# Kernel optimization log

Measured on AMD Instinct MI355X. Metric: run time of the kernel, lower is better.

## Reference

```python
import jax, jax.numpy as jnp
import numpy as np

D = 65
CHUNK = 64
K = 64
SCALE = D ** (-0.5)

def gelu(x):
    return jax.nn.gelu(x, approximate=False)  # torch nn.GELU default is exact erf

def setup_inputs() -> dict:
    key = jax.random.key(0)
    ks = jax.random.split(key, 16)
    B, N = 32, 16384
    s = SCALE
    return {
        "x": jax.random.normal(ks[0], (B, N, D), jnp.float32),
        # query_gen: Linear(D,D) -> GELU -> Linear(D, K*D)
        "Wq1": jax.random.normal(ks[1], (D, D), jnp.float32) * s,
        "bq1": jnp.zeros((D,), jnp.float32),
        "Wq2": jax.random.normal(ks[2], (D, K * D), jnp.float32) * s,
        "bq2": jnp.zeros((K * D,), jnp.float32),
        "Wk": jax.random.normal(ks[3], (D, D), jnp.float32) * s,
        "bk": jnp.zeros((D,), jnp.float32),
        "Wv": jax.random.normal(ks[4], (D, D), jnp.float32) * s,
        "bv": jnp.zeros((D,), jnp.float32),
        "cross_q": jax.random.normal(ks[5], (1, D), jnp.float32) * s,
        "pos_enc": jax.random.normal(ks[6], (1, CHUNK, D), jnp.float32) * s,
        "Wr": jax.random.normal(ks[7], (D, D), jnp.float32) * (1.0 / np.sqrt(D)),
        "br": jnp.zeros((D,), jnp.float32),
        "gamma": jnp.ones((D,), jnp.float32),
        "beta": jnp.zeros((D,), jnp.float32),
    }

def reference(x, Wq1, bq1, Wq2, bq2, Wk, bk, Wv, bv, cross_q, pos_enc, Wr, br, gamma, beta):
    B, N, d = x.shape
    nb = N // CHUNK  # N chosen divisible by CHUNK -> mask is all True, pad branch skipped

    # global average (mask all-ones => plain mean over N)
    gavg = jnp.mean(x, axis=1)  # [B, D]

    # queries: MLP on global average, reshape to [B, K, D], scaled
    q = (gelu(gavg @ Wq1 + bq1) @ Wq2 + bq2).reshape(B, K, d) * SCALE

    # keys / values: Linear + GELU, chunked, + positional encoding per chunk
    keys = gelu(x @ Wk + bk).reshape(B, nb, CHUNK, d) + pos_enc[None]      # [B,nb,C,D]
    values = gelu(x @ Wv + bv).reshape(B, nb, CHUNK, d) + pos_enc[None]    # [B,nb,C,D]

    # block-local attention (mask is all-True, masked_fill is a no-op)
    scores = jnp.einsum('bkd,bncd->bnkc', q, keys) * SCALE                 # [B,nb,K,C]
    w = jax.nn.softmax(scores, axis=-1)                                    # dropout = eval-mode identity
    blk = jnp.einsum('bnkc,bncd->bnkd', w, values)                         # [B,nb,K,D]
    blk = jnp.transpose(blk, (0, 2, 1, 3))                                 # [B,K,nb,D]

    # cross-block attention with a single learned query
    cs = jnp.einsum('d,bknd->bkn', cross_q[0], blk) * SCALE                # [B,K,nb]
    cw = jax.nn.softmax(cs, axis=-1)
    compressed = jnp.einsum('bkn,bknd->bkd', cw, blk)                      # [B,K,D]

    # residual + LayerNorm
    compressed = compressed + (gavg @ Wr + br)[:, None, :]
    mu = jnp.mean(compressed, axis=-1, keepdims=True)
    var = jnp.var(compressed, axis=-1, keepdims=True)
    return (compressed - mu) * jax.lax.rsqrt(var + 1e-5) * gamma + beta
```

## Files before the change

### kernel.cpp

```cpp
#include <hip/hip_runtime.h>
#include <hip/hip_bf16.h>

#define BATCH 32
#define NSEQ  16384
#define DDIM  65
#define CHUNK 64
#define KQ    64
#define NBLK  256
#define SCALE 0.12403473458920847f

typedef __bf16 bf16x8 __attribute__((ext_vector_type(8)));
typedef float  f32x4  __attribute__((ext_vector_type(4)));
#define MFMA16(a, b, c) __builtin_amdgcn_mfma_f32_16x16x32_bf16(a, b, c, 0, 0, 0)

#define BLK_ROWSTRIDE 72
#define BLK_CHUNKSTRIDE (64 * 72)
#define BLK_BSTRIDE ((size_t)NBLK * 64 * 72)

__device__ __forceinline__ float gelu_exact(float v) {
    return 0.5f * v * (1.0f + erff(v * 0.7071067811865476f));
}

__device__ __forceinline__ float gelu_tanh(float x) {
    float x2 = x * x;
    float t  = 0.7978845608028654f * x * fmaf(0.044715f, x2, 1.0f);
    float e  = __expf(2.0f * t);
    float th = 1.0f - 2.0f * __builtin_amdgcn_rcpf(e + 1.0f);
    return 0.5f * x * (1.0f + th);
}

__global__ __launch_bounds__(320) void k_gavg(const float* __restrict__ x,
                                              float* __restrict__ partial,
                                              const float* __restrict__ Wk,
                                              const float* __restrict__ Wv,
                                              __bf16* __restrict__ WkT,
                                              __bf16* __restrict__ WvT) {
    const int tid = threadIdx.x;
    if (blockIdx.y == 32) {
        const int i = blockIdx.x * 320 + tid;
        const int m = i / 5120;
        const int j = i - m * 5120;
        const int d = j >> 6, e = j & 63;
        const float* W = m ? Wv : Wk;
        __bf16* T = m ? WvT : WkT;
        T[(size_t)d * 64 + e] = (d < DDIM) ? (__bf16)W[e * DDIM + d]
                                           : (__bf16)0.0f;
        return;
    }
    const int s = blockIdx.x;
    const int b = blockIdx.y;
    const int g = tid / 65;
    const int j = tid - g * 65;
    const bool active = tid < 260;
    float acc[4] = {0.f, 0.f, 0.f, 0.f};
    if (active) {
        const float4* p = (const float4*)(x + (size_t)b * NSEQ * DDIM
                                            + (size_t)s * 512 * DDIM);
        #pragma unroll 8
        for (int it = 0; it < 32; ++it) {
            const float4 v = p[(it * 4 + g) * 65 + j];
            acc[0] += v.x; acc[1] += v.y; acc[2] += v.z; acc[3] += v.w;
        }
    }
    __shared__ float lds[4][65][4];
    if (active) {
        lds[g][j][0] = acc[0]; lds[g][j][1] = acc[1];
        lds[g][j][2] = acc[2]; lds[g][j][3] = acc[3];
    }
    __syncthreads();
    if (tid < DDIM) {
        float a = 0.f;
        #pragma unroll
        for (int rr = 0; rr < 4; ++rr) {
            const int f = tid + 65 * rr;
            const int jj = f >> 2, ee = f & 3;
            a += lds[0][jj][ee] + lds[1][jj][ee]
               + lds[2][jj][ee] + lds[3][jj][ee];
        }
        partial[((size_t)b * 32 + s) * DDIM + tid] = a;
    }
}

__global__ __launch_bounds__(256) void k_qgen1(const float* __restrict__ partial,
    const float* __restrict__ Wq1, const float* __restrict__ bq1,
    const float* __restrict__ Wr,  const float* __restrict__ br,
    float* __restrict__ h_out, float* __restrict__ r_out) {
    const int b = blockIdx.x, tid = threadIdx.x;
    __shared__ float g[DDIM];
    if (tid < DDIM) {
        float a = 0.f;
        const float* p = partial + (size_t)b * 32 * DDIM + tid;
        #pragma unroll 8
        for (int s = 0; s < 32; ++s) a += p[s * DDIM];
        g[tid] = a * (1.0f / 16384.0f);
    }
    __syncthreads();
    if (tid < DDIM) {
        float a = bq1[tid];
        for (int e = 0; e < DDIM; ++e) a += g[e] * Wq1[e * DDIM + tid];
        h_out[b * DDIM + tid] = gelu_exact(a);
    } else if (tid >= 128 && tid < 128 + DDIM) {
        const int d = tid - 128;
        float a = br[d];
        for (int e = 0; e < DDIM; ++e) a += g[e] * Wr[e * DDIM + d];
        r_out[b * DDIM + d] = a;
    }
}

__global__ __launch_bounds__(256) void k_qgen2(const float* __restrict__ h_in,
    const float* __restrict__ Wq2, const float* __restrict__ bq2,
    __bf16* __restrict__ qbf, float* __restrict__ q64) {
    const int b = blockIdx.y, tid = threadIdx.x;
    const int o = blockIdx.x * 256 + tid;
    __shared__ float h[DDIM];
    if (tid < DDIM) h[tid] = h_in[b * DDIM + tid];
    __syncthreads();
    if (o >= KQ * DDIM) return;
    float a = bq2[o];
    #pragma unroll 13
    for (int e = 0; e < DDIM; ++e) a += h[e] * Wq2[e * (KQ * DDIM) + o];
    a *= SCALE;
    const int k = o / DDIM, d = o - k * DDIM;
    if (d < 64) qbf[(size_t)b * 4096 + k * 64 + d] = (__bf16)a;
    else        q64[b * 64 + k] = a;
}

__global__ __launch_bounds__(256) void k_attn(const float* __restrict__ x,
    const __bf16* __restrict__ qbf, const float* __restrict__ q64,
    const __bf16* __restrict__ WkT, const __bf16* __restrict__ WvT,
    const float* __restrict__ Wk, const float* __restrict__ bkb,
    const float* __restrict__ Wv, const float* __restrict__ bvb,
    const float* __restrict__ pos, const float* __restrict__ cq,
    __bf16* __restrict__ blk_out, float* __restrict__ cs_out) {
    const int nb = blockIdx.x;
    const int b  = blockIdx.y;
    const int tid = threadIdx.x;
    const int lane = tid & 63, w = tid >> 6;
    const int l16 = lane & 15, quad = lane >> 4;

    __shared__ __align__(16) __bf16 keys[64 * 72];
    __shared__ __align__(16) __bf16 valsT[64 * 72];
    __shared__ float vals64[64];
    __shared__ float xs64[64];

    __bf16* blk_row = blk_out + (size_t)b * BLK_BSTRIDE
                              + (size_t)nb * BLK_CHUNKSTRIDE;

    float wk64v[5], wv64v[5], bkv[5], bvv[5], posv[5][4];
    {
        #pragma unroll
        for (int nt = 0; nt < 5; ++nt) {
            const int d = nt * 16 + l16;
            const int dc = d > 64 ? 64 : d;
            wk64v[nt] = Wk[64 * DDIM + dc];
            wv64v[nt] = Wv[64 * DDIM + dc];
            bkv[nt]   = bkb[dc];
            bvv[nt]   = bvb[dc];
            #pragma unroll
            for (int r = 0; r < 4; ++r)
                posv[nt][r] = pos[(w * 16 + quad * 4 + r) * DDIM + dc];
        }
    }

    {
        const int c = tid >> 2, g = tid & 3;
        const float* xrow = x + ((size_t)b * NSEQ + (size_t)nb * CHUNK + c) * DDIM;
        __bf16* dst = keys + c * 72;
        #pragma unroll
        for (int j = 0; j < 16; ++j)
            dst[g + 4 * j] = (__bf16)xrow[g + 4 * j];
        if (g == 0) xs64[c] = xrow[64];
    }
    __syncthreads();

    {
        const __bf16* arow = keys + (w * 16 + l16) * 72 + quad * 8;
        bf16x8 a0 = *(const bf16x8*)arow;
        bf16x8 a1 = *(const bf16x8*)(arow + 32);
        f32x4 ak[5], av[5];
        const f32x4 z = {0.f, 0.f, 0.f, 0.f};
        #pragma unroll
        for (int nt = 0; nt < 5; ++nt) {
            const __bf16* bkr = WkT + (nt * 16 + l16) * 64 + quad * 8;
            const __bf16* bvr = WvT + (nt * 16 + l16) * 64 + quad * 8;
            ak[nt] = MFMA16(a0, *(const bf16x8*)bkr, z);
            ak[nt] = MFMA16(a1, *(const bf16x8*)(bkr + 32), ak[nt]);
            av[nt] = MFMA16(a0, *(const bf16x8*)bvr, z);
            av[nt] = MFMA16(a1, *(const bf16x8*)(bvr + 32), av[nt]);
        }
        const float4 xe4 = *(const float4*)(xs64 + w * 16 + quad * 4);
        const float xe[4] = {xe4.x, xe4.y, xe4.z, xe4.w};
        #pragma unroll
        for (int nt = 0; nt < 5; ++nt) {
            const int d = nt * 16 + l16;
            if (d <= 64) {
                #pragma unroll
                for (int r = 0; r < 4; ++r) {
                    const int c = w * 16 + quad * 4 + r;
                    const float pv = posv[nt][r];
                    const float kvv = gelu_tanh(fmaf(xe[r], wk64v[nt], ak[nt][r]) + bkv[nt]) + pv;
                    const float vvv = gelu_tanh(fmaf(xe[r], wv64v[nt], av[nt][r]) + bvv[nt]) + pv;
                    keys[c * 72 + d] = (__bf16)kvv;
                    if (d < 64) valsT[d * 72 + c] = (__bf16)vvv;
                    else        vals64[c] = vvv;
                }
            }
        }
    }
    __syncthreads();

    float st[4][4];
    float inv[4];
    {
        const __bf16* aq = qbf + (size_t)b * 4096 + (w * 16 + l16) * 64 + quad * 8;
        bf16x8 qa0 = *(const bf16x8*)aq;
        bf16x8 qa1 = *(const bf16x8*)(aq + 32);
        const f32x4 z = {0.f, 0.f, 0.f, 0.f};
        const float4 q4 = *(const float4*)(q64 + b * 64 + w * 16 + quad * 4);
        const float q64k[4] = {q4.x, q4.y, q4.z, q4.w};
        #pragma unroll
        for (int nt = 0; nt < 4; ++nt) {
            const __bf16* kb = keys + (nt * 16 + l16) * 72 + quad * 8;
            f32x4 sacc = MFMA16(qa0, *(const bf16x8*)kb, z);
            sacc = MFMA16(qa1, *(const bf16x8*)(kb + 32), sacc);
            const float k64c = (float)keys[(nt * 16 + l16) * 72 + 64];
            #pragma unroll
            for (int r = 0; r < 4; ++r)
                st[nt][r] = fmaf(q64k[r], k64c, sacc[r]) * SCALE;
        }
        float mr[4], sum[4];
        #pragma unroll
        for (int r = 0; r < 4; ++r) {
            float m = fmaxf(fmaxf(st[0][r], st[1][r]), fmaxf(st[2][r], st[3][r]));
            m = fmaxf(m, __shfl_xor(m, 1));
            m = fmaxf(m, __shfl_xor(m, 2));
            m = fmaxf(m, __shfl_xor(m, 4));
            m = fmaxf(m, __shfl_xor(m, 8));
            mr[r] = m;
            sum[r] = 0.f;
        }
        #pragma unroll
        for (int nt = 0; nt < 4; ++nt)
            #pragma unroll
            for (int r = 0; r < 4; ++r) {
                st[nt][r] = __expf(st[nt][r] - mr[r]);
                sum[r] += st[nt][r];
            }
        #pragma unroll
        for (int r = 0; r < 4; ++r) {
            float s = sum[r];
            s += __shfl_xor(s, 1);
            s += __shfl_xor(s, 2);
            s += __shfl_xor(s, 4);
            s += __shfl_xor(s, 8);
            inv[r] = __builtin_amdgcn_rcpf(s);
        }
    }
    __syncthreads();

    float csr[4];
    {
        #pragma unroll
        for (int nt = 0; nt < 4; ++nt)
            #pragma unroll
            for (int r = 0; r < 4; ++r)
                keys[(w * 16 + quad * 4 + r) * 72 + nt * 16 + l16] =
                    (__bf16)(st[nt][r] * inv[r]);
        float v64l[4];
        #pragma unroll
        for (int nt = 0; nt < 4; ++nt) v64l[nt] = vals64[nt * 16 + l16];
        const float cq64 = cq[64];
        #pragma unroll
        for (int r = 0; r < 4; ++r) {
            float o = st[0][r] * v64l[0];
            o = fmaf(st[1][r], v64l[1], o);
            o = fmaf(st[2][r], v64l[2], o);
            o = fmaf(st[3][r], v64l[3], o);
            o += __shfl_xor(o, 1);
            o += __shfl_xor(o, 2);
            o += __shfl_xor(o, 4);
            o += __shfl_xor(o, 8);
            csr[r] = 0.f;
            if (l16 == 0) {
                const float o64 = o * inv[r];
                const int k = w * 16 + quad * 4 + r;
                bf16x8 v8;
                #pragma unroll
                for (int i2 = 0; i2 < 8; ++i2) v8[i2] = (__bf16)0.0f;
                v8[0] = (__bf16)o64;
                *(bf16x8*)(blk_row + k * BLK_ROWSTRIDE + 64) = v8;
                csr[r] = o64 * cq64;
            }
        }
    }

    {
        const __bf16* pr = keys + (w * 16 + l16) * 72 + quad * 8;
        bf16x8 pa0 = *(const bf16x8*)pr;
        bf16x8 pa1 = *(const bf16x8*)(pr + 32);
        const f32x4 z = {0.f, 0.f, 0.f, 0.f};
        #pragma unroll
        for (int nt = 0; nt < 4; ++nt) {
            const __bf16* vb = valsT + (nt * 16 + l16) * 72 + quad * 8;
            f32x4 o = MFMA16(pa0, *(const bf16x8*)vb, z);
            o = MFMA16(pa1, *(const bf16x8*)(vb + 32), o);
            const int d = nt * 16 + l16;
            const float cqd = cq[d];
            #pragma unroll
            for (int r = 0; r < 4; ++r) {
                const int k = w * 16 + quad * 4 + r;
                blk_row[k * BLK_ROWSTRIDE + d] = (__bf16)o[r];
                csr[r] = fmaf(o[r], cqd, csr[r]);
            }
        }
        #pragma unroll
        for (int r = 0; r < 4; ++r) {
            float v = csr[r];
            v += __shfl_xor(v, 1);
            v += __shfl_xor(v, 2);
            v += __shfl_xor(v, 4);
            v += __shfl_xor(v, 8);
            if (l16 == 0) {
                const int k = w * 16 + quad * 4 + r;
                cs_out[((size_t)b * KQ + k) * NBLK + nb] = v * SCALE;
            }
        }
    }
}

__global__ __launch_bounds__(256) void k_cross(
    const __bf16* __restrict__ blk, const float* __restrict__ cs,
    const float* __restrict__ rres, const float* __restrict__ gamma,
    const float* __restrict__ beta, float* __restrict__ out) {
    const int bk_ = blockIdx.x;
    const int b = bk_ >> 6, k = bk_ & 63;
    const int tid = threadIdx.x;
    const int w = tid >> 6, lane = tid & 63;

    __shared__ float ew[NBLK];
    __shared__ float wredA[4];
    __shared__ float lred[252][8];
    __shared__ float vv[DDIM];
    __shared__ float stats[2];

    const float v = cs[(size_t)bk_ * NBLK + tid];
    float m = v;
    for (int off = 32; off; off >>= 1) m = fmaxf(m, __shfl_down(m, off));
    if (lane == 0) wredA[w] = m;
    __syncthreads();
    m = fmaxf(fmaxf(wredA[0], wredA[1]), fmaxf(wredA[2], wredA[3]));
    const float e = __expf(v - m);
    ew[tid] = e;
    float s = e;
    for (int off = 32; off; off >>= 1) s += __shfl_down(s, off);
    __syncthreads();
    if (lane == 0) wredA[w] = s;
    __syncthreads();
    const float inv = 1.0f / (wredA[0] + wredA[1] + wredA[2] + wredA[3]);

    const int g = tid / 9, seg = tid - g * 9;
    float acc[8] = {0.f, 0.f, 0.f, 0.f, 0.f, 0.f, 0.f, 0.f};
    if (tid < 252) {
        const __bf16* base = blk + (size_t)b * BLK_BSTRIDE
                                 + k * BLK_ROWSTRIDE + seg * 8;
        #pragma unroll 2
        for (int it = 0; it < 10; ++it) {
            const int r = it * 28 + g;
            if (r < NBLK) {
                bf16x8 vx = *(const bf16x8*)(base + (size_t)r * BLK_CHUNKSTRIDE);
                const float wg = ew[r];
                #pragma unroll
                for (int i2 = 0; i2 < 8; ++i2)
                    acc[i2] = fmaf(wg, (float)vx[i2], acc[i2]);
            }
        }
        #pragma unroll
        for (int i2 = 0; i2 < 8; ++i2) lred[tid][i2] = acc[i2];
    }
    __syncthreads();
    if (tid < 72) {
        const int sg = tid >> 3, i2 = tid & 7;
        float a = 0.f;
        #pragma unroll 7
        for (int gg = 0; gg < 28; ++gg) a += lred[gg * 9 + sg][i2];
        const int d = sg * 8 + i2;
        if (d < DDIM) vv[d] = a * inv + rres[b * DDIM + d];
    }
    __syncthreads();
    if (tid < 64) {
        float a  = vv[tid] + (tid == 0 ? vv[64] : 0.f);
        float sq = vv[tid] * vv[tid] + (tid == 0 ? vv[64] * vv[64] : 0.f);
        for (int off = 32; off; off >>= 1) {
            a  += __shfl_down(a, off);
            sq += __shfl_down(sq, off);
        }
        if (tid == 0) {
            const float mu  = a * (1.0f / DDIM);
            const float var = sq * (1.0f / DDIM) - mu * mu;
            stats[0] = mu;
            stats[1] = rsqrtf(var + 1e-5f);
        }
    }
    __syncthreads();
    if (tid < DDIM) {
        out[(size_t)bk_ * DDIM + tid] =
            (vv[tid] - stats[0]) * stats[1] * gamma[tid] + beta[tid];
    }
}

extern "C" void kernel_launch(void* const* d_in, const int* in_sizes, int n_in,
                              void* d_out, int out_size, void* d_ws, size_t ws_size,
                              hipStream_t stream) {
    const float* x    = (const float*)d_in[0];
    const float* Wq1  = (const float*)d_in[1];
    const float* bq1  = (const float*)d_in[2];
    const float* Wq2  = (const float*)d_in[3];
    const float* bq2  = (const float*)d_in[4];
    const float* Wk   = (const float*)d_in[5];
    const float* bk   = (const float*)d_in[6];
    const float* Wv   = (const float*)d_in[7];
    const float* bv   = (const float*)d_in[8];
    const float* cq   = (const float*)d_in[9];
    const float* pos  = (const float*)d_in[10];
    const float* Wr   = (const float*)d_in[11];
    const float* br   = (const float*)d_in[12];
    const float* gamma= (const float*)d_in[13];
    const float* beta = (const float*)d_in[14];
    float* out = (float*)d_out;

    char* w8 = (char*)d_ws;
    __bf16* blk     = (__bf16*)w8;
    float*  partial = (float*)w8;
    float*  rres    = (float*)(w8 + 75497472);
    float*  q64     = (float*)(w8 + 75505792);
    float*  hbuf    = (float*)(w8 + 75513984);
    float*  cs      = (float*)(w8 + 75522304);
    __bf16* qbf     = (__bf16*)(w8 + 77619456);
    __bf16* WkT     = (__bf16*)(w8 + 77881600);
    __bf16* WvT     = (__bf16*)(w8 + 77891840);

    k_gavg<<<dim3(32, 33), 320, 0, stream>>>(x, partial, Wk, Wv, WkT, WvT);
    k_qgen1<<<BATCH, 256, 0, stream>>>(partial, Wq1, bq1, Wr, br, hbuf, rres);
    k_qgen2<<<dim3(17, BATCH), 256, 0, stream>>>(hbuf, Wq2, bq2, qbf, q64);
    k_attn<<<dim3(NBLK, BATCH), 256, 0, stream>>>(x, qbf, q64, WkT, WvT,
                                                  Wk, bk, Wv, bv, pos, cq,
                                                  blk, cs);
    k_cross<<<BATCH * KQ, 256, 0, stream>>>(blk, cs, rres, gamma, beta, out);
}
```

Measured before the change: 380.9 us.

## Coalesce x loads with float4 and stage block output through LDS

The chunk of x is now read as contiguous float4 vectors and scattered into the bf16 LDS tile, replacing strided per-element loads. The block attention output is staged in shared memory (reusing valsT) and then written to global memory with coalesced 16-byte vector stores instead of scattered 2-byte stores. cross_q values are hoisted into registers. This adds two extra barriers and index arithmetic with divide-by-65 tricks.

```diff
diff --git a/kernel.cpp b/kernel.cpp
--- a/kernel.cpp
+++ b/kernel.cpp
@@ -146,7 +146,8 @@
     __bf16* blk_row = blk_out + (size_t)b * BLK_BSTRIDE
                               + (size_t)nb * BLK_CHUNKSTRIDE;
 
-    float wk64v[5], wv64v[5], bkv[5], bvv[5], posv[5][4];
+    float wk64v[5], wv64v[5], bkv[5], bvv[5], posv[5][4], cqv[4];
+    float cq64;
     {
         #pragma unroll
         for (int nt = 0; nt < 5; ++nt) {
@@ -160,16 +161,30 @@
             for (int r = 0; r < 4; ++r)
                 posv[nt][r] = pos[(w * 16 + quad * 4 + r) * DDIM + dc];
         }
-    }
-
-    {
-        const int c = tid >> 2, g = tid & 3;
-        const float* xrow = x + ((size_t)b * NSEQ + (size_t)nb * CHUNK + c) * DDIM;
-        __bf16* dst = keys + c * 72;
-        #pragma unroll
-        for (int j = 0; j < 16; ++j)
-            dst[g + 4 * j] = (__bf16)xrow[g + 4 * j];
-        if (g == 0) xs64[c] = xrow[64];
+        #pragma unroll
+        for (int nt = 0; nt < 4; ++nt) cqv[nt] = cq[nt * 16 + l16];
+        cq64 = cq[64];
+    }
+
+    {
+        const float4* xf4 = (const float4*)(x + ((size_t)b * NSEQ
+                                                 + (size_t)nb * CHUNK) * DDIM);
+        #pragma unroll
+        for (int ii = 0; ii < 5; ++ii) {
+            const int F = ii * 256 + tid;
+            if (ii < 4 || tid < 16) {
+                const float4 v = xf4[F];
+                const int idx0 = 4 * F;
+                int c = (idx0 * 4033) >> 18;
+                int e = idx0 - c * 65;
+                const float vv[4] = {v.x, v.y, v.z, v.w};
+                #pragma unroll
+                for (int i = 0; i < 4; ++i) {
+                    if (e == 64) { xs64[c] = vv[i]; c += 1; e = 0; }
+                    else         { keys[c * 72 + e] = (__bf16)vv[i]; e += 1; }
+                }
+            }
+        }
     }
     __syncthreads();
 
@@ -258,7 +273,7 @@
     }
     __syncthreads();
 
-    float csr[4];
+    float csr[4], o64r[4];
     {
         #pragma unroll
         for (int nt = 0; nt < 4; ++nt)
@@ -269,7 +284,6 @@
         float v64l[4];
         #pragma unroll
         for (int nt = 0; nt < 4; ++nt) v64l[nt] = vals64[nt * 16 + l16];
-        const float cq64 = cq[64];
         #pragma unroll
         for (int r = 0; r < 4; ++r) {
             float o = st[0][r] * v64l[0];
@@ -280,37 +294,49 @@
             o += __shfl_xor(o, 2);
             o += __shfl_xor(o, 4);
             o += __shfl_xor(o, 8);
-            csr[r] = 0.f;
+            o64r[r] = 0.f;
+            csr[r]  = 0.f;
             if (l16 == 0) {
-                const float o64 = o * inv[r];
+                o64r[r] = o * inv[r];
+                csr[r]  = o64r[r] * cq64;
+            }
+        }
+    }
+
+    {
+        const __bf16* pr = keys + (w * 16 + l16) * 72 + quad * 8;
+        bf16x8 pa0 = *(const bf16x8*)pr;
+        bf16x8 pa1 = *(const bf16x8*)(pr + 32);
+        const f32x4 z = {0.f, 0.f, 0.f, 0.f};
+        f32x4 o[4];
+        #pragma unroll
+        for (int nt = 0; nt < 4; ++nt) {
+            const __bf16* vb = valsT + (nt * 16 + l16) * 72 + quad * 8;
+            o[nt] = MFMA16(pa0, *(const bf16x8*)vb, z);
+            o[nt] = MFMA16(pa1, *(const bf16x8*)(vb + 32), o[nt]);
+        }
+        __syncthreads();
+        __bf16* outl = valsT;
+        #pragma unroll
+        for (int nt = 0; nt < 4; ++nt) {
+            const int d = nt * 16 + l16;
+            const float cqd = cqv[nt];
+            #pragma unroll
+            for (int r = 0; r < 4; ++r) {
+                const int k = w * 16 + quad * 4 + r;
+                outl[k * 72 + d] = (__bf16)o[nt][r];
+                csr[r] = fmaf(o[nt][r], cqd, csr[r]);
+            }
+        }
+        if (l16 == 0) {
+            #pragma unroll
+            for (int r = 0; r < 4; ++r) {
                 const int k = w * 16 + quad * 4 + r;
                 bf16x8 v8;
                 #pragma unroll
                 for (int i2 = 0; i2 < 8; ++i2) v8[i2] = (__bf16)0.0f;
-                v8[0] = (__bf16)o64;
-                *(bf16x8*)(blk_row + k * BLK_ROWSTRIDE + 64) = v8;
-                csr[r] = o64 * cq64;
-            }
-        }
-    }
-
-    {
-        const __bf16* pr = keys + (w * 16 + l16) * 72 + quad * 8;
-        bf16x8 pa0 = *(const bf16x8*)pr;
-        bf16x8 pa1 = *(const bf16x8*)(pr + 32);
-        const f32x4 z = {0.f, 0.f, 0.f, 0.f};
-        #pragma unroll
-        for (int nt = 0; nt < 4; ++nt) {
-            const __bf16* vb = valsT + (nt * 16 + l16) * 72 + quad * 8;
-            f32x4 o = MFMA16(pa0, *(const bf16x8*)vb, z);
-            o = MFMA16(pa1, *(const bf16x8*)(vb + 32), o);
-            const int d = nt * 16 + l16;
-            const float cqd = cq[d];
-            #pragma unroll
-            for (int r = 0; r < 4; ++r) {
-                const int k = w * 16 + quad * 4 + r;
-                blk_row[k * BLK_ROWSTRIDE + d] = (__bf16)o[r];
-                csr[r] = fmaf(o[r], cqd, csr[r]);
+                v8[0] = (__bf16)o64r[r];
+                *(bf16x8*)(outl + k * 72 + 64) = v8;
             }
         }
         #pragma unroll
@@ -325,6 +351,12 @@
                 cs_out[((size_t)b * KQ + k) * NBLK + nb] = v * SCALE;
             }
         }
+        __syncthreads();
+        const bf16x8* src = (const bf16x8*)outl;
+        bf16x8* dst = (bf16x8*)blk_row;
+        dst[tid]       = src[tid];
+        dst[tid + 256] = src[tid + 256];
+        if (tid < 64) dst[tid + 512] = src[tid + 512];
     }
 }
 
```

Result: no change. 382.4 us (+0.4%).

## Process one chunk per wavefront in attention kernel to remove block barriers

Applied to the files above, without the earlier changes.

The attention kernel now gives each 64-lane wavefront a whole 64-token chunk, with two chunks per 128-thread block, instead of splitting one chunk over four wavefronts. Each wave loops over four 16-row tiles, so all __syncthreads barriers disappear and only wave-private LDS is used. x is loaded straight from global memory into MFMA operand registers rather than staged through shared memory. In exchange each wave does four times the serial work and holds a 64-entry score array in registers, which may raise register pressure and reduce occupancy or latency hiding.

```diff
diff --git a/kernel.cpp b/kernel.cpp
--- a/kernel.cpp
+++ b/kernel.cpp
@@ -27,6 +27,12 @@
     float e  = __expf(2.0f * t);
     float th = 1.0f - 2.0f * __builtin_amdgcn_rcpf(e + 1.0f);
     return 0.5f * x * (1.0f + th);
+}
+
+__device__ __forceinline__ f32x4 ld4u(const float* p) {
+    f32x4 v;
+    __builtin_memcpy(&v, p, 16);
+    return v;
 }
 
 __global__ __launch_bounds__(320) void k_gavg(const float* __restrict__ x,
@@ -125,113 +131,119 @@
     else        q64[b * 64 + k] = a;
 }
 
-__global__ __launch_bounds__(256) void k_attn(const float* __restrict__ x,
+__global__ __launch_bounds__(128) void k_attn(const float* __restrict__ x,
     const __bf16* __restrict__ qbf, const float* __restrict__ q64,
     const __bf16* __restrict__ WkT, const __bf16* __restrict__ WvT,
     const float* __restrict__ Wk, const float* __restrict__ bkb,
     const float* __restrict__ Wv, const float* __restrict__ bvb,
     const float* __restrict__ pos, const float* __restrict__ cq,
     __bf16* __restrict__ blk_out, float* __restrict__ cs_out) {
-    const int nb = blockIdx.x;
-    const int b  = blockIdx.y;
-    const int tid = threadIdx.x;
-    const int lane = tid & 63, w = tid >> 6;
-    const int l16 = lane & 15, quad = lane >> 4;
-
-    __shared__ __align__(16) __bf16 keys[64 * 72];
-    __shared__ __align__(16) __bf16 valsT[64 * 72];
-    __shared__ float vals64[64];
-    __shared__ float xs64[64];
-
+    const int tid  = threadIdx.x;
+    const int w    = tid >> 6, lane = tid & 63;
+    const int l16  = lane & 15, quad = lane >> 4;
+    const int nb   = blockIdx.x * 2 + w;
+    const int b    = blockIdx.y;
+
+    __shared__ __align__(16) __bf16 ksh[2][64 * 72];
+    __shared__ __align__(16) __bf16 vsh[2][64 * 72];
+    __shared__ float v64sh[2][64];
+    __bf16* K   = ksh[w];
+    __bf16* VT  = vsh[w];
+    float*  V64 = v64sh[w];
+
+    const float* xc = x + ((size_t)b * NSEQ + (size_t)nb * CHUNK) * DDIM;
     __bf16* blk_row = blk_out + (size_t)b * BLK_BSTRIDE
                               + (size_t)nb * BLK_CHUNKSTRIDE;
-
-    float wk64v[5], wv64v[5], bkv[5], bvv[5], posv[5][4];
-    {
+    const f32x4 z = {0.f, 0.f, 0.f, 0.f};
+
+    float wk64v[5], wv64v[5], bkv[5], bvv[5], cqv[4];
+    #pragma unroll
+    for (int nt = 0; nt < 5; ++nt) {
+        const int d  = nt * 16 + l16;
+        const int dc = d > 64 ? 64 : d;
+        wk64v[nt] = Wk[64 * DDIM + dc];
+        wv64v[nt] = Wv[64 * DDIM + dc];
+        bkv[nt]   = bkb[dc];
+        bvv[nt]   = bvb[dc];
+    }
+    #pragma unroll
+    for (int nt = 0; nt < 4; ++nt) cqv[nt] = cq[nt * 16 + l16];
+    const float cq64 = cq[64];
+
+    #pragma unroll
+    for (int mt = 0; mt < 4; ++mt) {
+        const float* xrow = xc + (mt * 16 + l16) * DDIM;
+        const f32x4 xa = ld4u(xrow + quad * 8);
+        const f32x4 xb = ld4u(xrow + quad * 8 + 4);
+        const f32x4 xc2 = ld4u(xrow + 32 + quad * 8);
+        const f32x4 xd = ld4u(xrow + 36 + quad * 8);
+        bf16x8 a0, a1;
+        #pragma unroll
+        for (int i = 0; i < 4; ++i) {
+            a0[i]     = (__bf16)xa[i];
+            a0[4 + i] = (__bf16)xb[i];
+            a1[i]     = (__bf16)xc2[i];
+            a1[4 + i] = (__bf16)xd[i];
+        }
+        f32x4 aK[5], aV[5];
         #pragma unroll
         for (int nt = 0; nt < 5; ++nt) {
-            const int d = nt * 16 + l16;
-            const int dc = d > 64 ? 64 : d;
-            wk64v[nt] = Wk[64 * DDIM + dc];
-            wv64v[nt] = Wv[64 * DDIM + dc];
-            bkv[nt]   = bkb[dc];
-            bvv[nt]   = bvb[dc];
-            #pragma unroll
-            for (int r = 0; r < 4; ++r)
-                posv[nt][r] = pos[(w * 16 + quad * 4 + r) * DDIM + dc];
-        }
-    }
-
-    {
-        const int c = tid >> 2, g = tid & 3;
-        const float* xrow = x + ((size_t)b * NSEQ + (size_t)nb * CHUNK + c) * DDIM;
-        __bf16* dst = keys + c * 72;
-        #pragma unroll
-        for (int j = 0; j < 16; ++j)
-            dst[g + 4 * j] = (__bf16)xrow[g + 4 * j];
-        if (g == 0) xs64[c] = xrow[64];
-    }
-    __syncthreads();
-
-    {
-        const __bf16* arow = keys + (w * 16 + l16) * 72 + quad * 8;
-        bf16x8 a0 = *(const bf16x8*)arow;
-        bf16x8 a1 = *(const bf16x8*)(arow + 32);
-        f32x4 ak[5], av[5];
-        const f32x4 z = {0.f, 0.f, 0.f, 0.f};
-        #pragma unroll
-        for (int nt = 0; nt < 5; ++nt) {
-            const __bf16* bkr = WkT + (nt * 16 + l16) * 64 + quad * 8;
-            const __bf16* bvr = WvT + (nt * 16 + l16) * 64 + quad * 8;
-            ak[nt] = MFMA16(a0, *(const bf16x8*)bkr, z);
-            ak[nt] = MFMA16(a1, *(const bf16x8*)(bkr + 32), ak[nt]);
-            av[nt] = MFMA16(a0, *(const bf16x8*)bvr, z);
-            av[nt] = MFMA16(a1, *(const bf16x8*)(bvr + 32), av[nt]);
-        }
-        const float4 xe4 = *(const float4*)(xs64 + w * 16 + quad * 4);
-        const float xe[4] = {xe4.x, xe4.y, xe4.z, xe4.w};
+            const __bf16* bk0 = WkT + (nt * 16 + l16) * 64 + quad * 8;
+            const __bf16* bv0 = WvT + (nt * 16 + l16) * 64 + quad * 8;
+            aK[nt] = MFMA16(a0, *(const bf16x8*)bk0, z);
+            aK[nt] = MFMA16(a1, *(const bf16x8*)(bk0 + 32), aK[nt]);
+            aV[nt] = MFMA16(a0, *(const bf16x8*)bv0, z);
+            aV[nt] = MFMA16(a1, *(const bf16x8*)(bv0 + 32), aV[nt]);
+        }
+        float xe[4];
+        #pragma unroll
+        for (int r = 0; r < 4; ++r)
+            xe[r] = xc[(mt * 16 + quad * 4 + r) * DDIM + 64];
         #pragma unroll
         for (int nt = 0; nt < 5; ++nt) {
             const int d = nt * 16 + l16;
             if (d <= 64) {
                 #pragma unroll
                 for (int r = 0; r < 4; ++r) {
-                    const int c = w * 16 + quad * 4 + r;
-                    const float pv = posv[nt][r];
-                    const float kvv = gelu_tanh(fmaf(xe[r], wk64v[nt], ak[nt][r]) + bkv[nt]) + pv;
-                    const float vvv = gelu_tanh(fmaf(xe[r], wv64v[nt], av[nt][r]) + bvv[nt]) + pv;
-                    keys[c * 72 + d] = (__bf16)kvv;
-                    if (d < 64) valsT[d * 72 + c] = (__bf16)vvv;
-                    else        vals64[c] = vvv;
+                    const int c = mt * 16 + quad * 4 + r;
+                    const float pv = pos[c * DDIM + d];
+                    const float kv = gelu_tanh(fmaf(xe[r], wk64v[nt], aK[nt][r]) + bkv[nt]) + pv;
+                    const float vv = gelu_tanh(fmaf(xe[r], wv64v[nt], aV[nt][r]) + bvv[nt]) + pv;
+                    K[c * 72 + d] = (__bf16)kv;
+                    if (d < 64) VT[d * 72 + c] = (__bf16)vv;
+                    else        V64[c] = vv;
                 }
             }
         }
     }
-    __syncthreads();
-
-    float st[4][4];
-    float inv[4];
-    {
-        const __bf16* aq = qbf + (size_t)b * 4096 + (w * 16 + l16) * 64 + quad * 8;
-        bf16x8 qa0 = *(const bf16x8*)aq;
-        bf16x8 qa1 = *(const bf16x8*)(aq + 32);
-        const f32x4 z = {0.f, 0.f, 0.f, 0.f};
-        const float4 q4 = *(const float4*)(q64 + b * 64 + w * 16 + quad * 4);
-        const float q64k[4] = {q4.x, q4.y, q4.z, q4.w};
-        #pragma unroll
-        for (int nt = 0; nt < 4; ++nt) {
-            const __bf16* kb = keys + (nt * 16 + l16) * 72 + quad * 8;
+
+    float st[4][4][4];
+    #pragma unroll
+    for (int mtk = 0; mtk < 4; ++mtk) {
+        const __bf16* aq = qbf + (size_t)b * 4096 + (mtk * 16 + l16) * 64 + quad * 8;
+        const bf16x8 qa0 = *(const bf16x8*)aq;
+        const bf16x8 qa1 = *(const bf16x8*)(aq + 32);
+        const f32x4 q4 = *(const f32x4*)(q64 + b * 64 + mtk * 16 + quad * 4);
+        #pragma unroll
+        for (int ntc = 0; ntc < 4; ++ntc) {
+            const __bf16* kb = K + (ntc * 16 + l16) * 72 + quad * 8;
             f32x4 sacc = MFMA16(qa0, *(const bf16x8*)kb, z);
             sacc = MFMA16(qa1, *(const bf16x8*)(kb + 32), sacc);
-            const float k64c = (float)keys[(nt * 16 + l16) * 72 + 64];
+            const float k64c = (float)K[(ntc * 16 + l16) * 72 + 64];
             #pragma unroll
             for (int r = 0; r < 4; ++r)
-                st[nt][r] = fmaf(q64k[r], k64c, sacc[r]) * SCALE;
-        }
-        float mr[4], sum[4];
+                st[mtk][ntc][r] = fmaf(q4[r], k64c, sacc[r]) * SCALE;
+        }
+    }
+
+    float o64r[4][4];
+    #pragma unroll
+    for (int mtk = 0; mtk < 4; ++mtk) {
+        float mr[4], sum[4], inv[4];
         #pragma unroll
         for (int r = 0; r < 4; ++r) {
-            float m = fmaxf(fmaxf(st[0][r], st[1][r]), fmaxf(st[2][r], st[3][r]));
+            float m = fmaxf(fmaxf(st[mtk][0][r], st[mtk][1][r]),
+                            fmaxf(st[mtk][2][r], st[mtk][3][r]));
             m = fmaxf(m, __shfl_xor(m, 1));
             m = fmaxf(m, __shfl_xor(m, 2));
             m = fmaxf(m, __shfl_xor(m, 4));
@@ -240,11 +252,11 @@
             sum[r] = 0.f;
         }
         #pragma unroll
-        for (int nt = 0; nt < 4; ++nt)
+        for (int ntc = 0; ntc < 4; ++ntc)
             #pragma unroll
             for (int r = 0; r < 4; ++r) {
-                st[nt][r] = __expf(st[nt][r] - mr[r]);
-                sum[r] += st[nt][r];
+                st[mtk][ntc][r] = __expf(st[mtk][ntc][r] - mr[r]);
+                sum[r] += st[mtk][ntc][r];
             }
         #pragma unroll
         for (int r = 0; r < 4; ++r) {
@@ -255,62 +267,61 @@
             s += __shfl_xor(s, 8);
             inv[r] = __builtin_amdgcn_rcpf(s);
         }
-    }
-    __syncthreads();
-
-    float csr[4];
-    {
-        #pragma unroll
-        for (int nt = 0; nt < 4; ++nt)
+        #pragma unroll
+        for (int ntc = 0; ntc < 4; ++ntc)
             #pragma unroll
             for (int r = 0; r < 4; ++r)
-                keys[(w * 16 + quad * 4 + r) * 72 + nt * 16 + l16] =
-                    (__bf16)(st[nt][r] * inv[r]);
+                K[(mtk * 16 + quad * 4 + r) * 72 + ntc * 16 + l16] =
+                    (__bf16)(st[mtk][ntc][r] * inv[r]);
         float v64l[4];
         #pragma unroll
-        for (int nt = 0; nt < 4; ++nt) v64l[nt] = vals64[nt * 16 + l16];
-        const float cq64 = cq[64];
+        for (int ntc = 0; ntc < 4; ++ntc) v64l[ntc] = V64[ntc * 16 + l16];
         #pragma unroll
         for (int r = 0; r < 4; ++r) {
-            float o = st[0][r] * v64l[0];
-            o = fmaf(st[1][r], v64l[1], o);
-            o = fmaf(st[2][r], v64l[2], o);
-            o = fmaf(st[3][r], v64l[3], o);
+            float o = st[mtk][0][r] * v64l[0];
+            o = fmaf(st[mtk][1][r], v64l[1], o);
+            o = fmaf(st[mtk][2][r], v64l[2], o);
+            o = fmaf(st[mtk][3][r], v64l[3], o);
             o += __shfl_xor(o, 1);
             o += __shfl_xor(o, 2);
             o += __shfl_xor(o, 4);
             o += __shfl_xor(o, 8);
-            csr[r] = 0.f;
-            if (l16 == 0) {
-                const float o64 = o * inv[r];
-                const int k = w * 16 + quad * 4 + r;
+            o64r[mtk][r] = (l16 == 0) ? o * inv[r] : 0.f;
+        }
+    }
+
+    #pragma unroll
+    for (int mtk = 0; mtk < 4; ++mtk) {
+        const __bf16* pr = K + (mtk * 16 + l16) * 72 + quad * 8;
+        const bf16x8 pa0 = *(const bf16x8*)pr;
+        const bf16x8 pa1 = *(const bf16x8*)(pr + 32);
+        float csr[4];
+        #pragma unroll
+        for (int r = 0; r < 4; ++r)
+            csr[r] = (l16 == 0) ? o64r[mtk][r] * cq64 : 0.f;
+        #pragma unroll
+        for (int nt = 0; nt < 4; ++nt) {
+            const __bf16* vb = VT + (nt * 16 + l16) * 72 + quad * 8;
+            f32x4 o = MFMA16(pa0, *(const bf16x8*)vb, z);
+            o = MFMA16(pa1, *(const bf16x8*)(vb + 32), o);
+            const int d = nt * 16 + l16;
+            const float cqd = cqv[nt];
+            #pragma unroll
+            for (int r = 0; r < 4; ++r) {
+                const int k = mtk * 16 + quad * 4 + r;
+                blk_row[k * BLK_ROWSTRIDE + d] = (__bf16)o[r];
+                csr[r] = fmaf(o[r], cqd, csr[r]);
+            }
+        }
+        if (l16 == 0) {
+            #pragma unroll
+            for (int r = 0; r < 4; ++r) {
+                const int k = mtk * 16 + quad * 4 + r;
                 bf16x8 v8;
                 #pragma unroll
                 for (int i2 = 0; i2 < 8; ++i2) v8[i2] = (__bf16)0.0f;
-                v8[0] = (__bf16)o64;
+                v8[0] = (__bf16)o64r[mtk][r];
                 *(bf16x8*)(blk_row + k * BLK_ROWSTRIDE + 64) = v8;
-                csr[r] = o64 * cq64;
-            }
-        }
-    }
-
-    {
-        const __bf16* pr = keys + (w * 16 + l16) * 72 + quad * 8;
-        bf16x8 pa0 = *(const bf16x8*)pr;
-        bf16x8 pa1 = *(const bf16x8*)(pr + 32);
-        const f32x4 z = {0.f, 0.f, 0.f, 0.f};
-        #pragma unroll
-        for (int nt = 0; nt < 4; ++nt) {
-            const __bf16* vb = valsT + (nt * 16 + l16) * 72 + quad * 8;
-            f32x4 o = MFMA16(pa0, *(const bf16x8*)vb, z);
-            o = MFMA16(pa1, *(const bf16x8*)(vb + 32), o);
-            const int d = nt * 16 + l16;
-            const float cqd = cq[d];
-            #pragma unroll
-            for (int r = 0; r < 4; ++r) {
-                const int k = w * 16 + quad * 4 + r;
-                blk_row[k * BLK_ROWSTRIDE + d] = (__bf16)o[r];
-                csr[r] = fmaf(o[r], cqd, csr[r]);
             }
         }
         #pragma unroll
@@ -321,7 +332,7 @@
             v += __shfl_xor(v, 4);
             v += __shfl_xor(v, 8);
             if (l16 == 0) {
-                const int k = w * 16 + quad * 4 + r;
+                const int k = mtk * 16 + quad * 4 + r;
                 cs_out[((size_t)b * KQ + k) * NBLK + nb] = v * SCALE;
             }
         }
@@ -442,8 +453,8 @@
     k_gavg<<<dim3(32, 33), 320, 0, stream>>>(x, partial, Wk, Wv, WkT, WvT);
     k_qgen1<<<BATCH, 256, 0, stream>>>(partial, Wq1, bq1, Wr, br, hbuf, rres);
     k_qgen2<<<dim3(17, BATCH), 256, 0, stream>>>(hbuf, Wq2, bq2, qbf, q64);
-    k_attn<<<dim3(NBLK, BATCH), 256, 0, stream>>>(x, qbf, q64, WkT, WvT,
-                                                  Wk, bk, Wv, bv, pos, cq,
-                                                  blk, cs);
+    k_attn<<<dim3(NBLK / 2, BATCH), 128, 0, stream>>>(x, qbf, q64, WkT, WvT,
+                                                      Wk, bk, Wv, bv, pos, cq,
+                                                      blk, cs);
     k_cross<<<BATCH * KQ, 256, 0, stream>>>(blk, cs, rres, gamma, beta, out);
 }
```

Measured after the change: 385.1 us. No clear change (+1.1%).
